# Optimization experiments

Hardware: AMD Instinct MI355X
Metric: run time of the kernel (lower is better)

Reference implementation:

```python
import jax, jax.numpy as jnp
import numpy as np

B, S, D, H, E, K = 2, 2048, 1024, 8, 4, 2
DH = D // H  # 128


def setup_inputs() -> dict:
    key = jax.random.key(0)
    ks = jax.random.split(key, 9)
    std = 1.0 / np.sqrt(D)
    return {
        "q_src": jax.random.normal(ks[0], (B, S, D), jnp.float32),
        "k_src": jax.random.normal(ks[1], (B, S, D), jnp.float32),
        "v_src": jax.random.normal(ks[2], (B, S, D), jnp.float32),
        "Wq": jax.random.normal(ks[3], (H * DH, D), jnp.float32) * std,
        "Wk": jax.random.normal(ks[4], (H * DH, D), jnp.float32) * std,
        "Wv": jax.random.normal(ks[5], (H, E, D, DH), jnp.float32) * std,   # per-head, per-expert V proj
        "Wo": jax.random.normal(ks[6], (H, E, DH, D), jnp.float32) * (1.0 / np.sqrt(H * DH)),
        "sel_v": jax.random.normal(ks[7], (H * E, D), jnp.float32) * std,   # V-expert router
        "sel_o": jax.random.normal(ks[8], (H * E, D), jnp.float32) * std,   # O-expert router
    }


def reference(q_src, k_src, v_src, Wq, Wk, Wv, Wo, sel_v, sel_o):
    s = DH ** -0.25  # scale.sqrt() applied to both q and k -> combined 1/sqrt(d_head)

    q = (q_src @ Wq.T * s).reshape(B, S, H, DH).transpose(0, 2, 1, 3)  # [B,H,S,DH]
    k = (k_src @ Wk.T * s).reshape(B, S, H, DH).transpose(0, 2, 1, 3)

    # --- V expert routing: sigmoid gate + top-k over experts, per head ---
    gv_all = jax.nn.sigmoid((k_src @ sel_v.T).reshape(B, S, H, E))
    gv, iv = jax.lax.top_k(gv_all, K)                                  # [B,S,H,K]
    # per-expert V projection (equiv. to CVMM grouped-GEMM), then gather selected experts
    v_all = jnp.einsum('bsd,hedk->bshek', v_src, Wv)                   # [B,S,H,E,DH]
    v = (jnp.take_along_axis(v_all, iv[..., None], axis=3) * gv[..., None]).sum(3)
    v = v.transpose(0, 2, 1, 3)                                        # [B,H,S,DH]

    # --- attention (mask=None; base class attend() is abstract, plain SDPA) ---
    scores = jnp.einsum('bhqd,bhkd->bhqk', q, k)
    att = jax.nn.softmax(scores, axis=-1)
    res = jnp.einsum('bhqk,bhkd->bhqd', att, v).transpose(0, 2, 1, 3)  # [B,S,H,DH]

    # --- O expert routing: weighted sum over heads and selected output experts ---
    go_all = jax.nn.sigmoid((q_src @ sel_o.T).reshape(B, S, H, E))
    go, io = jax.lax.top_k(go_all, K)                                  # [B,S,H,K]
    gd = (go[..., None] * jax.nn.one_hot(io, E, dtype=res.dtype)).sum(-2)  # dense gates [B,S,H,E]
    gated = res[:, :, :, None, :] * gd[..., None]                      # [B,S,H,E,DH]
    out = jnp.einsum('bshed,hedo->bso', gated, Wo)                     # [B,S,D]
    return out
```

## Files before the change

### kernel.cpp

```cpp
#include <hip/hip_runtime.h>

#define BB 2
#define SS 2048
#define DD 1024
#define HH 8
#define EE 4
#define DHH 128
#define RR (BB*SS)

typedef __attribute__((ext_vector_type(8))) short short8;
typedef __attribute__((ext_vector_type(4))) short short4v;
typedef __attribute__((ext_vector_type(4))) float f32x4;

__device__ __forceinline__ float b2f(short x) {
    unsigned u = ((unsigned)(unsigned short)x) << 16;
    return __uint_as_float(u);
}
__device__ __forceinline__ short f2bf(float f) {
    unsigned u = __float_as_uint(f);
    unsigned r = (u + 0x7fffu + ((u >> 16) & 1u)) >> 16;
    return (short)(unsigned short)r;
}

__device__ __forceinline__ void gl_lds16(const short* g, short* l) {
    __builtin_amdgcn_global_load_lds(
        (const __attribute__((address_space(1))) unsigned int*)g,
        (__attribute__((address_space(3))) unsigned int*)l,
        16, 0, 0);
}

template <bool BF16_OUT>
__device__ __forceinline__ void gemm16_body(
    short* As, short* Bs,
    const short* __restrict__ A, const short* __restrict__ Bm, void* __restrict__ Cv,
    int Kd, int lda, int ldb, int ldc, float alpha, int bm0, int bn0)
{
    const int t = threadIdx.x;
    const int lane = t & 63, wave = t >> 6;
    const int lm = lane & 15, quad = lane >> 4;
    const int wm = (wave >> 1) * 64, wn = (wave & 1) * 64;
    f32x4 acc[4][4] = {};

    const int srow = t >> 2, scol = (t & 3) * 8;
    const short* Ag = A + (long)(bm0 + srow) * lda + scol;
    const short* Bg = Bm + (long)(bn0 + srow) * ldb + scol;
    const long ldaH = (long)lda * 64, ldbH = (long)ldb * 64;
    short* Asd = As + srow * 32 + scol;
    short* Bsd = Bs + srow * 32 + scol;

    for (int k0 = 0; k0 < Kd; k0 += 32) {
        __syncthreads();
        gl_lds16(Ag + k0,        Asd);
        gl_lds16(Ag + k0 + ldaH, Asd + 64 * 32);
        gl_lds16(Bg + k0,        Bsd);
        gl_lds16(Bg + k0 + ldbH, Bsd + 64 * 32);
        __syncthreads();

        short8 af[4], bf[4];
#pragma unroll
        for (int i = 0; i < 4; i++)
            af[i] = *(const short8*)&As[(wm + i * 16 + lm) * 32 + quad * 8];
#pragma unroll
        for (int j = 0; j < 4; j++)
            bf[j] = *(const short8*)&Bs[(wn + j * 16 + lm) * 32 + quad * 8];
#pragma unroll
        for (int i = 0; i < 4; i++)
#pragma unroll
            for (int j = 0; j < 4; j++)
                acc[i][j] = __builtin_amdgcn_mfma_f32_16x16x32_bf16(
                    af[i], bf[j], acc[i][j], 0, 0, 0);
    }
#pragma unroll
    for (int i = 0; i < 4; i++) {
#pragma unroll
        for (int j = 0; j < 4; j++) {
            int n = bn0 + wn + j * 16 + lm;
#pragma unroll
            for (int r = 0; r < 4; r++) {
                int m = bm0 + wm + i * 16 + quad * 4 + r;
                float v = acc[i][j][r] * alpha;
                if (BF16_OUT) ((short*)Cv)[(long)m * ldc + n] = f2bf(v);
                else          ((float*)Cv)[(long)m * ldc + n] = v;
            }
        }
    }
}

__global__ __launch_bounds__(256)
void shc_gemm_bt16(const short* __restrict__ A, const short* __restrict__ Bm,
                   void* __restrict__ Cv, int Kd, int lda, int ldb, int ldc,
                   float alpha)
{
    __shared__ short As[128 * 32];
    __shared__ short Bs[128 * 32];
    gemm16_body<true>(As, Bs, A, Bm, Cv, Kd, lda, ldb, ldc, alpha,
                      blockIdx.y * 128, blockIdx.x * 128);
}

__global__ __launch_bounds__(256)
void shc_gemm_qk(const short* __restrict__ Qs, const short* __restrict__ Ks,
                 const short* __restrict__ Wq16, const short* __restrict__ Wk16,
                 short* __restrict__ Qo, short* __restrict__ Ko, float alpha)
{
    __shared__ short As[128 * 32];
    __shared__ short Bs[128 * 32];
    if (blockIdx.z == 0)
        gemm16_body<true>(As, Bs, Qs, Wq16, Qo, 1024, 1024, 1024, 1024,
                          alpha, blockIdx.y * 128, blockIdx.x * 128);
    else
        gemm16_body<true>(As, Bs, Ks, Wk16, Ko, 1024, 1024, 1024, 1024,
                          alpha, blockIdx.y * 128, blockIdx.x * 128);
}

__global__ __launch_bounds__(256)
void shc_gemm_out(const short* __restrict__ X, const short* __restrict__ WoT,
                  float* __restrict__ out, float* __restrict__ P1)
{
    __shared__ short As[128 * 32];
    __shared__ short Bs[128 * 32];
    const int koff = blockIdx.z * 2048;
    float* C = blockIdx.z ? P1 : out;
    gemm16_body<false>(As, Bs, X + koff, WoT + koff, C,
                       2048, 4096, 4096, 1024, 1.0f,
                       blockIdx.y * 128, blockIdx.x * 128);
}

__global__ __launch_bounds__(256)
void shc_add(float* __restrict__ out, const float* __restrict__ P1)
{
    long i = ((long)blockIdx.x * 256 + threadIdx.x) * 4;
    f32x4 a = *(const f32x4*)(out + i);
    f32x4 b = *(const f32x4*)(P1 + i);
#pragma unroll
    for (int j = 0; j < 4; j++) a[j] += b[j];
    *(f32x4*)(out + i) = a;
}

__global__ __launch_bounds__(256)
void shc_cvt3(const float* __restrict__ a, const float* __restrict__ b,
              const float* __restrict__ c, short* __restrict__ oa,
              short* __restrict__ ob, short* __restrict__ oc)
{
    const float* src = blockIdx.z == 0 ? a : (blockIdx.z == 1 ? b : c);
    short* dst       = blockIdx.z == 0 ? oa : (blockIdx.z == 1 ? ob : oc);
    long i = ((long)blockIdx.x * 256 + threadIdx.x) * 8;
    f32x4 f0 = *(const f32x4*)(src + i);
    f32x4 f1 = *(const f32x4*)(src + i + 4);
    short8 o;
#pragma unroll
    for (int j = 0; j < 4; j++) {
        o[j]     = f2bf(f0[j]);
        o[4 + j] = f2bf(f1[j]);
    }
    *(short8*)(dst + i) = o;
}

__global__ __launch_bounds__(256)
void shc_gates4(const float* __restrict__ q_src, const float* __restrict__ k_src,
                const float* __restrict__ sel_v, const float* __restrict__ sel_o,
                float* __restrict__ gv_d, float* __restrict__ go_d)
{
    const int t = threadIdx.x, lane = t & 63, wave = t >> 6;
    const int bid = blockIdx.x;
    const int s = bid & 1;
    const int r0 = (bid >> 1) * 8 + wave * 2;
    const float* srcb = s ? q_src : k_src;
    const float* selb = s ? sel_o : sel_v;

    double S0[16], S1[16];
#pragma unroll
    for (int i = 0; i < 4; i++) {
        f32x4 v0 = *(const f32x4*)(srcb + (long)r0 * 1024 + lane * 16 + i * 4);
        f32x4 v1 = *(const f32x4*)(srcb + (long)(r0 + 1) * 1024 + lane * 16 + i * 4);
#pragma unroll
        for (int j = 0; j < 4; j++) {
            S0[i * 4 + j] = (double)v0[j];
            S1[i * 4 + j] = (double)v1[j];
        }
    }

    float myv = 0.f;
#pragma unroll 2
    for (int o = 0; o < 32; ++o) {
        f32x4 W[4];
#pragma unroll
        for (int i = 0; i < 4; i++)
            W[i] = *(const f32x4*)(selb + o * 1024 + lane * 16 + i * 4);
        double a0 = 0.0, a1 = 0.0;
#pragma unroll
        for (int i = 0; i < 4; i++)
#pragma unroll
            for (int j = 0; j < 4; j++) {
                double w = (double)W[i][j];
                a0 += S0[i * 4 + j] * w;
                a1 += S1[i * 4 + j] * w;
            }
        a0 += __shfl_xor(a0, 1);  a1 += __shfl_xor(a1, 1);
        a0 += __shfl_xor(a0, 2);  a1 += __shfl_xor(a1, 2);
        a0 += __shfl_xor(a0, 4);  a1 += __shfl_xor(a1, 4);
        a0 += __shfl_xor(a0, 8);  a1 += __shfl_xor(a1, 8);
        a0 += __shfl_xor(a0, 16); a1 += __shfl_xor(a1, 16);
        double tcross = (lane < 32) ? a1 : a0;
        double u = __shfl_xor(tcross, 32);
        double tot = ((lane < 32) ? a0 : a1) + u;
        myv = ((lane & 31) == o) ? (float)tot : myv;
    }

    float sg = 1.f / (1.f + __expf(-myv));
    float g1 = __shfl_xor(sg, 1);
    float g2 = __shfl_xor(sg, 2);
    float g3 = __shfl_xor(sg, 3);
    const int e = lane & 3;
    int rank = 0;
    rank += (g1 > sg) || (g1 == sg && (e ^ 1) < e);
    rank += (g2 > sg) || (g2 == sg && (e ^ 2) < e);
    rank += (g3 > sg) || (g3 == sg && (e ^ 3) < e);
    const long row = r0 + (lane >> 5);
    float* outp = (s ? go_d : gv_d) + row * 32 + (lane & 31);
    *outp = (rank < 2) ? sg : 0.f;
}

__global__ __launch_bounds__(256)
void shc_transpose_w(const float* __restrict__ Wv, short* __restrict__ WvT,
                     const float* __restrict__ Wo, short* __restrict__ WoT)
{
    __shared__ float Ls[32][33];
    const int t = threadIdx.x;
    const int rr = t >> 3, cc = (t & 7) * 4;
    const int bid = blockIdx.x;
    if (bid < 4096) {
        const int dhT = bid & 3, dT = (bid >> 2) & 31, he = bid >> 7;
        const int d0 = dT * 32, dh0 = dhT * 32;
        f32x4 vin = *(const f32x4*)(Wv + (long)(he * 1024 + d0 + rr) * 128 + dh0 + cc);
#pragma unroll
        for (int j = 0; j < 4; j++) Ls[rr][cc + j] = vin[j];
        __syncthreads();
        short4v ov;
#pragma unroll
        for (int j = 0; j < 4; j++) ov[j] = f2bf(Ls[cc + j][rr]);
        *(short4v*)(WvT + (long)(he * 128 + dh0 + rr) * 1024 + d0 + cc) = ov;
    } else {
        const int b2 = bid - 4096;
        const int oT = b2 & 31, kT = b2 >> 5;
        const int k0 = kT * 32, o0 = oT * 32;
        f32x4 vin = *(const f32x4*)(Wo + (long)(k0 + rr) * 1024 + o0 + cc);
#pragma unroll
        for (int j = 0; j < 4; j++) Ls[rr][cc + j] = vin[j];
        __syncthreads();
        short4v ov;
#pragma unroll
        for (int j = 0; j < 4; j++) ov[j] = f2bf(Ls[cc + j][rr]);
        *(short4v*)(WoT + (long)(o0 + rr) * 4096 + k0 + cc) = ov;
    }
}

__global__ __launch_bounds__(256)
void shc_combine_vt(const short* __restrict__ v_all, const float* __restrict__ gv_d,
                    short* __restrict__ Vt)
{
    __shared__ short Ls[64 * 136];
    const int t = threadIdx.x;
    const int blk = blockIdx.x;
    const int st = blk & 31, h = (blk >> 5) & 7, b = blk >> 8;
    const int s0 = st * 64;
    const int sl = t >> 2, dh0 = (t & 3) * 32;
    const long row = (long)(b * SS) + s0 + sl;
    const float* g = gv_d + row * 32 + h * 4;
    float g0 = g[0], g1 = g[1], g2 = g[2], g3 = g[3];
    const short* va = v_all + row * 4096 + h * 512;
#pragma unroll
    for (int j = 0; j < 4; j++) {
        int dh = dh0 + j * 8;
        short8 e0 = *(const short8*)(va + 0 * 128 + dh);
        short8 e1 = *(const short8*)(va + 1 * 128 + dh);
        short8 e2 = *(const short8*)(va + 2 * 128 + dh);
        short8 e3 = *(const short8*)(va + 3 * 128 + dh);
        short8 outv;
#pragma unroll
        for (int i = 0; i < 8; i++)
            outv[i] = f2bf(g0 * b2f(e0[i]) + g1 * b2f(e1[i])
                         + g2 * b2f(e2[i]) + g3 * b2f(e3[i]));
        *(short8*)&Ls[sl * 136 + dh] = outv;
    }
    __syncthreads();
    const int dh = t >> 1, sc0 = (t & 1) * 32;
    short* op = Vt + ((long)(b * HH + h) * DHH + dh) * SS + s0 + sc0;
#pragma unroll
    for (int j = 0; j < 4; j++) {
        short8 ov;
#pragma unroll
        for (int i = 0; i < 8; i++)
            ov[i] = Ls[(sc0 + j * 8 + i) * 136 + dh];
        *(short8*)(op + j * 8) = ov;
    }
}

#define NEG10L2E -14.426950408889634f
__global__ __launch_bounds__(256, 1)
void shc_attn_mfma(const short* __restrict__ Q, const short* __restrict__ Kg,
                   const short* __restrict__ Vt, const float* __restrict__ go_d,
                   short* __restrict__ X)
{
    __shared__ __align__(16) char smem[49152];
    short* Ks = (short*)smem;
    short* Vs = (short*)(smem + 16384);
    const int t = threadIdx.x;
    const int lane = t & 63, wave = t >> 6;
    const int lm = lane & 15, quad = lane >> 4;
    short* Pw = (short*)(smem + 32768) + wave * 2048;
    const int blk = blockIdx.x;
    const int qt = blk & 15, h = (blk >> 4) & 7, b = blk >> 7;
    const int q0 = qt * 128 + wave * 32;
    const short* Qb = Q + ((long)(b * SS) + q0) * DD + h * DHH;
    const short* Kb = Kg + (long)(b * SS) * DD + h * DHH;
    const short* Vb = Vt + (long)(b * HH + h) * DHH * SS;

    short8 af[2][4];
#pragma unroll
    for (int qb = 0; qb < 2; qb++)
#pragma unroll
        for (int c = 0; c < 4; c++)
            af[qb][c] = *(const short8*)(Qb + (long)(qb * 16 + lm) * DD + c * 32 + quad * 8);

    f32x4 o_acc[2][8] = {};
    float l_lane[2][4] = {};

    const int lmswz = (lm & 7) << 3;
    const int w16 = wave * 16, w32 = wave * 32;

    const int rK = lane >> 4;
    const int colKe = ((lane & 15) * 8) ^ (rK << 3);
    const int colKo = colKe ^ 32;
    const int rV = lane >> 3;
    const int colV = ((lane & 7) * 8) ^ (rV << 3);

    for (int kt = 0; kt < SS / 64; ++kt) {
        __syncthreads();
#pragma unroll
        for (int i = 0; i < 4; i++) {
            const short* kg = Kb + (long)(kt * 64 + w16 + i * 4 + rK) * DD
                              + ((i & 1) ? colKo : colKe);
            gl_lds16(kg, Ks + (w16 + i * 4) * 128);
            const short* vg = Vb + (long)(w32 + i * 8 + rV) * SS + kt * 64 + colV;
            gl_lds16(vg, Vs + (w32 + i * 8) * 64);
        }
        __syncthreads();

#pragma unroll
        for (int f = 0; f < 4; f++) {
            f32x4 a0 = {NEG10L2E, NEG10L2E, NEG10L2E, NEG10L2E};
            f32x4 a1 = a0;
#pragma unroll
            for (int c = 0; c < 4; c++) {
                short8 bf = *(const short8*)&Ks[(f * 16 + lm) * 128
                                                + ((c * 32 + quad * 8) ^ lmswz)];
                a0 = __builtin_amdgcn_mfma_f32_16x16x32_bf16(af[0][c], bf, a0, 0, 0, 0);
                a1 = __builtin_amdgcn_mfma_f32_16x16x32_bf16(af[1][c], bf, a1, 0, 0, 0);
            }
#pragma unroll
            for (int r = 0; r < 4; r++) {
                const int pr = quad * 4 + r;
                const int psw = (pr & 7) << 3;
                float p0 = exp2f(a0[r]);
                l_lane[0][r] += p0;
                Pw[pr * 64 + ((f * 16 + lm) ^ psw)] = f2bf(p0);
                float p1 = exp2f(a1[r]);
                l_lane[1][r] += p1;
                Pw[(16 + pr) * 64 + ((f * 16 + lm) ^ psw)] = f2bf(p1);
            }
        }

        short8 ap[2][2];
#pragma unroll
        for (int qb = 0; qb < 2; qb++) {
            ap[qb][0] = *(const short8*)&Pw[(qb * 16 + lm) * 64 + ((quad * 8) ^ lmswz)];
            ap[qb][1] = *(const short8*)&Pw[(qb * 16 + lm) * 64 + ((32 + quad * 8) ^ lmswz)];
        }
#pragma unroll
        for (int d = 0; d < 8; d++) {
            short8 bv0 = *(const short8*)&Vs[(d * 16 + lm) * 64 + ((quad * 8) ^ lmswz)];
            short8 bv1 = *(const short8*)&Vs[(d * 16 + lm) * 64 + ((32 + quad * 8) ^ lmswz)];
            o_acc[0][d] = __builtin_amdgcn_mfma_f32_16x16x32_bf16(ap[0][0], bv0, o_acc[0][d], 0, 0, 0);
            o_acc[0][d] = __builtin_amdgcn_mfma_f32_16x16x32_bf16(ap[0][1], bv1, o_acc[0][d], 0, 0, 0);
            o_acc[1][d] = __builtin_amdgcn_mfma_f32_16x16x32_bf16(ap[1][0], bv0, o_acc[1][d], 0, 0, 0);
            o_acc[1][d] = __builtin_amdgcn_mfma_f32_16x16x32_bf16(ap[1][1], bv1, o_acc[1][d], 0, 0, 0);
        }
    }

    float inv_r[2][4];
#pragma unroll
    for (int qb = 0; qb < 2; qb++)
#pragma unroll
        for (int r = 0; r < 4; r++) {
            float l = l_lane[qb][r];
            l += __shfl_xor(l, 1);
            l += __shfl_xor(l, 2);
            l += __shfl_xor(l, 4);
            l += __shfl_xor(l, 8);
            inv_r[qb][r] = 1.f / l;
        }

    float* Of = (float*)smem;
#pragma unroll
    for (int hb = 0; hb < 2; hb++) {
        __syncthreads();
#pragma unroll
        for (int r = 0; r < 4; r++) {
#pragma unroll
            for (int d = 0; d < 8; d++)
                Of[(w16 + quad * 4 + r) * 132 + d * 16 + lm] = o_acc[hb][d][r] * inv_r[hb][r];
        }
        __syncthreads();
        const int xr = t >> 2, xc0 = (t & 3) * 8;
        const long grow = (long)(b * SS) + qt * 128 + (xr >> 4) * 32 + hb * 16 + (xr & 15);
        const float* go4 = go_d + grow * 32 + h * 4;
        float gg[4] = {go4[0], go4[1], go4[2], go4[3]};
        short* Xp = X + grow * 4096 + h * 512;
#pragma unroll
        for (int e = 0; e < 4; e++) {
#pragma unroll
            for (int j = 0; j < 4; j++) {
                int c = xc0 + 32 * j;
                f32x4 f0 = *(const f32x4*)&Of[xr * 132 + c];
                f32x4 f1 = *(const f32x4*)&Of[xr * 132 + c + 4];
                short8 s;
#pragma unroll
                for (int i = 0; i < 4; i++) {
                    s[i]     = f2bf(f0[i] * gg[e]);
                    s[4 + i] = f2bf(f1[i] * gg[e]);
                }
                *(short8*)(Xp + e * 128 + c) = s;
            }
        }
    }
}

extern "C" void kernel_launch(void* const* d_in, const int* in_sizes, int n_in,
                              void* d_out, int out_size, void* d_ws, size_t ws_size,
                              hipStream_t stream)
{
    const float* q_src = (const float*)d_in[0];
    const float* k_src = (const float*)d_in[1];
    const float* v_src = (const float*)d_in[2];
    const float* Wq    = (const float*)d_in[3];
    const float* Wk    = (const float*)d_in[4];
    const float* Wv    = (const float*)d_in[5];
    const float* Wo    = (const float*)d_in[6];
    const float* sel_v = (const float*)d_in[7];
    const float* sel_o = (const float*)d_in[8];
    float* out = (float*)d_out;
    char* ws = (char*)d_ws;

    short* Qb16 = (short*)(ws + 0);
    short* Kb16 = (short*)(ws + 8388608);
    short* Vtg  = (short*)(ws + 16777216);
    short* Vs16 = (short*)(ws + 16777216);
    short* Vall = (short*)(ws + 25165824);
    short* X    = (short*)(ws + 25165824);
    short* Wq16 = (short*)(ws + 25165824);
    short* Wk16 = (short*)(ws + 27262976);
    float* P1   = (float*)(ws + 58720256);
    short* Qs16 = (short*)(ws + 58720256);
    short* Ks16 = (short*)(ws + 67108864);
    short* WvT  = (short*)(ws + 75497472);
    short* WoT  = (short*)(ws + 83886080);
    float* GVd  = (float*)(ws + 92274688);
    float* GOd  = (float*)(ws + 92798976);

    const float s_scale = 0.29730177875068026f * 1.2011224087864498f;

    dim3 blk(256);
    shc_cvt3<<<dim3(2048, 1, 3), blk, 0, stream>>>(q_src, k_src, v_src, Qs16, Ks16, Vs16);
    shc_cvt3<<<dim3(512, 1, 2), blk, 0, stream>>>(Wq, Wk, Wk, Wq16, Wk16, Wk16);
    shc_gemm_qk<<<dim3(8, 32, 2), blk, 0, stream>>>(Qs16, Ks16, Wq16, Wk16, Qb16, Kb16, s_scale);
    shc_gates4<<<1024, blk, 0, stream>>>(q_src, k_src, sel_v, sel_o, GVd, GOd);
    shc_transpose_w<<<8192, blk, 0, stream>>>(Wv, WvT, Wo, WoT);
    shc_gemm_bt16<<<dim3(32, 32), blk, 0, stream>>>(Vs16, WvT, Vall, 1024, 1024, 1024, 4096, 1.0f);
    shc_combine_vt<<<512, blk, 0, stream>>>(Vall, GVd, Vtg);
    shc_attn_mfma<<<256, blk, 0, stream>>>(Qb16, Kb16, Vtg, GOd, X);
    shc_gemm_out<<<dim3(8, 32, 2), blk, 0, stream>>>(X, WoT, out, P1);
    shc_add<<<4096, blk, 0, stream>>>(out, P1);
}
```

Measured before the change: 426.4 us.

## Double-buffer K/V tiles and split attention into smaller two-wave blocks

The attention kernel now prefetches the next K/V tile into a second LDS buffer while the current tile is being computed, which removes one barrier per iteration and hides global-load latency. Blocks shrink from 4 waves and 128 queries to 2 waves and 64 queries, doubling the grid to 512 blocks. The epilogue is reorganised for the new block shape. In exchange, LDS per block grows to 72KB and each wave issues twice as many staging loads.

```diff
diff --git a/kernel.cpp b/kernel.cpp
--- a/kernel.cpp
+++ b/kernel.cpp
@@ -296,21 +296,19 @@
 }
 
 #define NEG10L2E -14.426950408889634f
-__global__ __launch_bounds__(256, 1)
+__global__ __launch_bounds__(128, 1)
 void shc_attn_mfma(const short* __restrict__ Q, const short* __restrict__ Kg,
                    const short* __restrict__ Vt, const float* __restrict__ go_d,
                    short* __restrict__ X)
 {
-    __shared__ __align__(16) char smem[49152];
-    short* Ks = (short*)smem;
-    short* Vs = (short*)(smem + 16384);
+    __shared__ __align__(16) char smem[73728];
     const int t = threadIdx.x;
     const int lane = t & 63, wave = t >> 6;
     const int lm = lane & 15, quad = lane >> 4;
-    short* Pw = (short*)(smem + 32768) + wave * 2048;
+    short* Pw = (short*)(smem + 65536) + wave * 2048;
     const int blk = blockIdx.x;
-    const int qt = blk & 15, h = (blk >> 4) & 7, b = blk >> 7;
-    const int q0 = qt * 128 + wave * 32;
+    const int qt = blk & 31, h = (blk >> 5) & 7, b = blk >> 8;
+    const int q0 = qt * 64 + wave * 32;
     const short* Qb = Q + ((long)(b * SS) + q0) * DD + h * DHH;
     const short* Kb = Kg + (long)(b * SS) * DD + h * DHH;
     const short* Vb = Vt + (long)(b * HH + h) * DHH * SS;
@@ -326,25 +324,33 @@
     float l_lane[2][4] = {};
 
     const int lmswz = (lm & 7) << 3;
-    const int w16 = wave * 16, w32 = wave * 32;
+    const int w32 = wave * 32, w64 = wave * 64;
 
     const int rK = lane >> 4;
-    const int colKe = ((lane & 15) * 8) ^ (rK << 3);
-    const int colKo = colKe ^ 32;
+    const int colK = ((lane & 15) * 8) ^ (rK << 3);
     const int rV = lane >> 3;
     const int colV = ((lane & 7) * 8) ^ (rV << 3);
 
+    auto STAGE = [&](int ktile, int bo) {
+        short* KsD = (short*)(smem + bo);
+        short* VsD = (short*)(smem + 16384 + bo);
+#pragma unroll
+        for (int i = 0; i < 8; i++) {
+            const short* kg = Kb + (long)(ktile * 64 + w32 + i * 4 + rK) * DD
+                              + (colK ^ ((i & 1) << 5));
+            gl_lds16(kg, KsD + (w32 + i * 4) * 128);
+            const short* vg = Vb + (long)(w64 + i * 8 + rV) * SS + ktile * 64 + colV;
+            gl_lds16(vg, VsD + (w64 + i * 8) * 64);
+        }
+    };
+
+    STAGE(0, 0);
     for (int kt = 0; kt < SS / 64; ++kt) {
+        const int bo = (kt & 1) << 15;
         __syncthreads();
-#pragma unroll
-        for (int i = 0; i < 4; i++) {
-            const short* kg = Kb + (long)(kt * 64 + w16 + i * 4 + rK) * DD
-                              + ((i & 1) ? colKo : colKe);
-            gl_lds16(kg, Ks + (w16 + i * 4) * 128);
-            const short* vg = Vb + (long)(w32 + i * 8 + rV) * SS + kt * 64 + colV;
-            gl_lds16(vg, Vs + (w32 + i * 8) * 64);
-        }
-        __syncthreads();
+        if (kt < SS / 64 - 1) STAGE(kt + 1, bo ^ 32768);
+        const short* Ks = (const short*)(smem + bo);
+        const short* Vs = (const short*)(smem + 16384 + bo);
 
 #pragma unroll
         for (int f = 0; f < 4; f++) {
@@ -401,36 +407,36 @@
         }
 
     float* Of = (float*)smem;
-#pragma unroll
-    for (int hb = 0; hb < 2; hb++) {
-        __syncthreads();
+    __syncthreads();
+#pragma unroll
+    for (int qb = 0; qb < 2; qb++)
 #pragma unroll
         for (int r = 0; r < 4; r++) {
 #pragma unroll
             for (int d = 0; d < 8; d++)
-                Of[(w16 + quad * 4 + r) * 132 + d * 16 + lm] = o_acc[hb][d][r] * inv_r[hb][r];
-        }
-        __syncthreads();
-        const int xr = t >> 2, xc0 = (t & 3) * 8;
-        const long grow = (long)(b * SS) + qt * 128 + (xr >> 4) * 32 + hb * 16 + (xr & 15);
-        const float* go4 = go_d + grow * 32 + h * 4;
-        float gg[4] = {go4[0], go4[1], go4[2], go4[3]};
-        short* Xp = X + grow * 4096 + h * 512;
-#pragma unroll
-        for (int e = 0; e < 4; e++) {
-#pragma unroll
-            for (int j = 0; j < 4; j++) {
-                int c = xc0 + 32 * j;
-                f32x4 f0 = *(const f32x4*)&Of[xr * 132 + c];
-                f32x4 f1 = *(const f32x4*)&Of[xr * 132 + c + 4];
-                short8 s;
-#pragma unroll
-                for (int i = 0; i < 4; i++) {
-                    s[i]     = f2bf(f0[i] * gg[e]);
-                    s[4 + i] = f2bf(f1[i] * gg[e]);
-                }
-                *(short8*)(Xp + e * 128 + c) = s;
+                Of[(w32 + qb * 16 + quad * 4 + r) * 132 + d * 16 + lm] =
+                    o_acc[qb][d][r] * inv_r[qb][r];
+        }
+    __syncthreads();
+    const int xr = t >> 1, xc0 = (t & 1) * 8;
+    const long grow = (long)(b * SS) + qt * 64 + xr;
+    const float* go4 = go_d + grow * 32 + h * 4;
+    float gg[4] = {go4[0], go4[1], go4[2], go4[3]};
+    short* Xp = X + grow * 4096 + h * 512;
+#pragma unroll
+    for (int e = 0; e < 4; e++) {
+#pragma unroll
+        for (int j = 0; j < 8; j++) {
+            int c = xc0 + 16 * j;
+            f32x4 f0 = *(const f32x4*)&Of[xr * 132 + c];
+            f32x4 f1 = *(const f32x4*)&Of[xr * 132 + c + 4];
+            short8 s;
+#pragma unroll
+            for (int i = 0; i < 4; i++) {
+                s[i]     = f2bf(f0[i] * gg[e]);
+                s[4 + i] = f2bf(f1[i] * gg[e]);
             }
+            *(short8*)(Xp + e * 128 + c) = s;
         }
     }
 }
@@ -477,7 +483,7 @@
     shc_transpose_w<<<8192, blk, 0, stream>>>(Wv, WvT, Wo, WoT);
     shc_gemm_bt16<<<dim3(32, 32), blk, 0, stream>>>(Vs16, WvT, Vall, 1024, 1024, 1024, 4096, 1.0f);
     shc_combine_vt<<<512, blk, 0, stream>>>(Vall, GVd, Vtg);
-    shc_attn_mfma<<<256, blk, 0, stream>>>(Qb16, Kb16, Vtg, GOd, X);
+    shc_attn_mfma<<<512, dim3(128), 0, stream>>>(Qb16, Kb16, Vtg, GOd, X);
     shc_gemm_out<<<dim3(8, 32, 2), blk, 0, stream>>>(X, WoT, out, P1);
     shc_add<<<4096, blk, 0, stream>>>(out, P1);
 }
```

Result: no change. 419.9 us (-1.5%).

## Split attention KV range across wave pairs and double grid size

Applied to the files above, without the earlier changes.

The attention kernel now processes 64 query rows per block instead of 128. The two wave pairs each handle half of the key/value sequence, and their partial outputs and row sums are merged through shared memory before the gated write. This doubles the block count from 256 to 512 to fill more compute units on the device, and the launch-bounds occupancy hint is relaxed. In exchange it uses more shared memory per block and adds a final reduction step. It also skips max-subtraction, which remains safe because the kernel relies on a fixed offset.

```diff
diff --git a/kernel.cpp b/kernel.cpp
--- a/kernel.cpp
+++ b/kernel.cpp
@@ -296,24 +296,26 @@
 }
 
 #define NEG10L2E -14.426950408889634f
-__global__ __launch_bounds__(256, 1)
+__global__ __launch_bounds__(256)
 void shc_attn_mfma(const short* __restrict__ Q, const short* __restrict__ Kg,
                    const short* __restrict__ Vt, const float* __restrict__ go_d,
                    short* __restrict__ X)
 {
-    __shared__ __align__(16) char smem[49152];
-    short* Ks = (short*)smem;
-    short* Vs = (short*)(smem + 16384);
+    __shared__ __align__(16) char smem[81920];
     const int t = threadIdx.x;
     const int lane = t & 63, wave = t >> 6;
     const int lm = lane & 15, quad = lane >> 4;
-    short* Pw = (short*)(smem + 32768) + wave * 2048;
+    const int wq = wave & 1;
+    const int wp = wave >> 1;
+    short* KsH = (short*)(smem + wp * 16384);
+    short* VsH = (short*)(smem + 32768 + wp * 16384);
+    short* Pw  = (short*)(smem + 65536) + wave * 2048;
     const int blk = blockIdx.x;
-    const int qt = blk & 15, h = (blk >> 4) & 7, b = blk >> 7;
-    const int q0 = qt * 128 + wave * 32;
+    const int qt = blk & 31, h = (blk >> 5) & 7, b = blk >> 8;
+    const int q0 = qt * 64 + wq * 32;
     const short* Qb = Q + ((long)(b * SS) + q0) * DD + h * DHH;
-    const short* Kb = Kg + (long)(b * SS) * DD + h * DHH;
-    const short* Vb = Vt + (long)(b * HH + h) * DHH * SS;
+    const short* Kb = Kg + (long)(b * SS + wp * 1024) * DD + h * DHH;
+    const short* Vb = Vt + (long)(b * HH + h) * DHH * SS + wp * 1024;
 
     short8 af[2][4];
 #pragma unroll
@@ -326,23 +328,21 @@
     float l_lane[2][4] = {};
 
     const int lmswz = (lm & 7) << 3;
-    const int w16 = wave * 16, w32 = wave * 32;
 
     const int rK = lane >> 4;
-    const int colKe = ((lane & 15) * 8) ^ (rK << 3);
-    const int colKo = colKe ^ 32;
+    const int colK = ((lane & 15) * 8) ^ (rK << 3);
     const int rV = lane >> 3;
     const int colV = ((lane & 7) * 8) ^ (rV << 3);
 
-    for (int kt = 0; kt < SS / 64; ++kt) {
-        __syncthreads();
-#pragma unroll
-        for (int i = 0; i < 4; i++) {
-            const short* kg = Kb + (long)(kt * 64 + w16 + i * 4 + rK) * DD
-                              + ((i & 1) ? colKo : colKe);
-            gl_lds16(kg, Ks + (w16 + i * 4) * 128);
-            const short* vg = Vb + (long)(w32 + i * 8 + rV) * SS + kt * 64 + colV;
-            gl_lds16(vg, Vs + (w32 + i * 8) * 64);
+    for (int kt = 0; kt < 16; ++kt) {
+        __syncthreads();
+#pragma unroll
+        for (int i = 0; i < 8; i++) {
+            const short* kg = Kb + (long)(kt * 64 + wq * 32 + i * 4 + rK) * DD
+                              + (colK ^ ((i & 1) << 5));
+            gl_lds16(kg, KsH + (wq * 32 + i * 4) * 128);
+            const short* vg = Vb + (long)(wq * 64 + i * 8 + rV) * SS + kt * 64 + colV;
+            gl_lds16(vg, VsH + (wq * 64 + i * 8) * 64);
         }
         __syncthreads();
 
@@ -352,8 +352,8 @@
             f32x4 a1 = a0;
 #pragma unroll
             for (int c = 0; c < 4; c++) {
-                short8 bf = *(const short8*)&Ks[(f * 16 + lm) * 128
-                                                + ((c * 32 + quad * 8) ^ lmswz)];
+                short8 bf = *(const short8*)&KsH[(f * 16 + lm) * 128
+                                                 + ((c * 32 + quad * 8) ^ lmswz)];
                 a0 = __builtin_amdgcn_mfma_f32_16x16x32_bf16(af[0][c], bf, a0, 0, 0, 0);
                 a1 = __builtin_amdgcn_mfma_f32_16x16x32_bf16(af[1][c], bf, a1, 0, 0, 0);
             }
@@ -378,8 +378,8 @@
         }
 #pragma unroll
         for (int d = 0; d < 8; d++) {
-            short8 bv0 = *(const short8*)&Vs[(d * 16 + lm) * 64 + ((quad * 8) ^ lmswz)];
-            short8 bv1 = *(const short8*)&Vs[(d * 16 + lm) * 64 + ((32 + quad * 8) ^ lmswz)];
+            short8 bv0 = *(const short8*)&VsH[(d * 16 + lm) * 64 + ((quad * 8) ^ lmswz)];
+            short8 bv1 = *(const short8*)&VsH[(d * 16 + lm) * 64 + ((32 + quad * 8) ^ lmswz)];
             o_acc[0][d] = __builtin_amdgcn_mfma_f32_16x16x32_bf16(ap[0][0], bv0, o_acc[0][d], 0, 0, 0);
             o_acc[0][d] = __builtin_amdgcn_mfma_f32_16x16x32_bf16(ap[0][1], bv1, o_acc[0][d], 0, 0, 0);
             o_acc[1][d] = __builtin_amdgcn_mfma_f32_16x16x32_bf16(ap[1][0], bv0, o_acc[1][d], 0, 0, 0);
@@ -387,7 +387,7 @@
         }
     }
 
-    float inv_r[2][4];
+    float lred[2][4];
 #pragma unroll
     for (int qb = 0; qb < 2; qb++)
 #pragma unroll
@@ -397,40 +397,55 @@
             l += __shfl_xor(l, 2);
             l += __shfl_xor(l, 4);
             l += __shfl_xor(l, 8);
-            inv_r[qb][r] = 1.f / l;
-        }
-
-    float* Of = (float*)smem;
-#pragma unroll
-    for (int hb = 0; hb < 2; hb++) {
-        __syncthreads();
+            lred[qb][r] = l;
+        }
+
+    __syncthreads();
+    float* Of0 = (float*)smem;
+    float* Of1 = (float*)(smem + 33792);
+    float* Lsum = (float*)(smem + 67584);
+    float* Ofp = wp ? Of1 : Of0;
+#pragma unroll
+    for (int qb = 0; qb < 2; qb++)
 #pragma unroll
         for (int r = 0; r < 4; r++) {
+            const int row = wq * 32 + qb * 16 + quad * 4 + r;
 #pragma unroll
             for (int d = 0; d < 8; d++)
-                Of[(w16 + quad * 4 + r) * 132 + d * 16 + lm] = o_acc[hb][d][r] * inv_r[hb][r];
-        }
-        __syncthreads();
-        const int xr = t >> 2, xc0 = (t & 3) * 8;
-        const long grow = (long)(b * SS) + qt * 128 + (xr >> 4) * 32 + hb * 16 + (xr & 15);
-        const float* go4 = go_d + grow * 32 + h * 4;
-        float gg[4] = {go4[0], go4[1], go4[2], go4[3]};
-        short* Xp = X + grow * 4096 + h * 512;
+                Ofp[row * 132 + d * 16 + lm] = o_acc[qb][d][r];
+            if (lm == 0) Lsum[wp * 64 + row] = lred[qb][r];
+        }
+    __syncthreads();
+    const int xr = t >> 2, xc0 = (t & 3) * 8;
+    const float inv = 1.f / (Lsum[xr] + Lsum[64 + xr]);
+    const long grow = (long)(b * SS) + qt * 64 + xr;
+    const float* go4 = go_d + grow * 32 + h * 4;
+    float gg[4];
+#pragma unroll
+    for (int e = 0; e < 4; e++) gg[e] = go4[e] * inv;
+    short* Xp = X + grow * 4096 + h * 512;
+#pragma unroll
+    for (int j = 0; j < 4; j++) {
+        int c = xc0 + 32 * j;
+        f32x4 u0a = *(const f32x4*)&Of0[xr * 132 + c];
+        f32x4 u0b = *(const f32x4*)&Of1[xr * 132 + c];
+        f32x4 u1a = *(const f32x4*)&Of0[xr * 132 + c + 4];
+        f32x4 u1b = *(const f32x4*)&Of1[xr * 132 + c + 4];
+        f32x4 u0, u1;
+#pragma unroll
+        for (int i = 0; i < 4; i++) {
+            u0[i] = u0a[i] + u0b[i];
+            u1[i] = u1a[i] + u1b[i];
+        }
 #pragma unroll
         for (int e = 0; e < 4; e++) {
-#pragma unroll
-            for (int j = 0; j < 4; j++) {
-                int c = xc0 + 32 * j;
-                f32x4 f0 = *(const f32x4*)&Of[xr * 132 + c];
-                f32x4 f1 = *(const f32x4*)&Of[xr * 132 + c + 4];
-                short8 s;
-#pragma unroll
-                for (int i = 0; i < 4; i++) {
-                    s[i]     = f2bf(f0[i] * gg[e]);
-                    s[4 + i] = f2bf(f1[i] * gg[e]);
-                }
-                *(short8*)(Xp + e * 128 + c) = s;
+            short8 s;
+#pragma unroll
+            for (int i = 0; i < 4; i++) {
+                s[i]     = f2bf(u0[i] * gg[e]);
+                s[4 + i] = f2bf(u1[i] * gg[e]);
             }
+            *(short8*)(Xp + e * 128 + c) = s;
         }
     }
 }
@@ -477,7 +492,7 @@
     shc_transpose_w<<<8192, blk, 0, stream>>>(Wv, WvT, Wo, WoT);
     shc_gemm_bt16<<<dim3(32, 32), blk, 0, stream>>>(Vs16, WvT, Vall, 1024, 1024, 1024, 4096, 1.0f);
     shc_combine_vt<<<512, blk, 0, stream>>>(Vall, GVd, Vtg);
-    shc_attn_mfma<<<256, blk, 0, stream>>>(Qb16, Kb16, Vtg, GOd, X);
+    shc_attn_mfma<<<512, blk, 0, stream>>>(Qb16, Kb16, Vtg, GOd, X);
     shc_gemm_out<<<dim3(8, 32, 2), blk, 0, stream>>>(X, WoT, out, P1);
     shc_add<<<4096, blk, 0, stream>>>(out, P1);
 }
```

After: 435.3 us. +2.1%, slower.
